# Optimization experiments

Measured on AMD Instinct MI355X. Metric: run time of the kernel, lower is better.

## Reference

```python
import jax, jax.numpy as jnp
import numpy as np

NUM_EXPERTS = 8
TOP_K = 2
INIT_STD = 0.02


def setup_inputs() -> dict:
    key = jax.random.key(0)
    ks = jax.random.split(key, 10)
    B, S, H, I, SI, E = 2, 512, 2048, 1408, 5632, NUM_EXPERTS
    return {
        "hidden_states": jax.random.normal(ks[0], (B, S, H), jnp.float32),
        "gate_w": jax.random.normal(ks[1], (H, E), jnp.float32) * INIT_STD,
        "w_gate": jax.random.normal(ks[2], (E, H, I), jnp.float32) * INIT_STD,
        "w_up": jax.random.normal(ks[3], (E, H, I), jnp.float32) * INIT_STD,
        "w_down": jax.random.normal(ks[4], (E, I, H), jnp.float32) * INIT_STD,
        "sw_gate": jax.random.normal(ks[5], (H, SI), jnp.float32) * INIT_STD,
        "sw_up": jax.random.normal(ks[6], (H, SI), jnp.float32) * INIT_STD,
        "sw_down": jax.random.normal(ks[7], (SI, H), jnp.float32) * INIT_STD,
        "shared_gate_w": jax.random.normal(ks[8], (H, 1), jnp.float32) * INIT_STD,
    }


def reference(hidden_states, gate_w, w_gate, w_up, w_down, sw_gate, sw_up, sw_down, shared_gate_w):
    # Router: logits [B,S,E] in float32, softmax, top-k (norm_topk_prob=False)
    router_logits = (hidden_states @ gate_w).astype(jnp.float32)
    routing_weights = jax.nn.softmax(router_logits, axis=-1)
    top_w, sel = jax.lax.top_k(routing_weights, TOP_K)  # [B,S,K]
    # Scatter top-k weights back to dense per-expert weights [B,S,E]
    # (equals sum_k (sel==e) * top_w, as in the original masked accumulation)
    w = (jax.nn.one_hot(sel, NUM_EXPERTS, dtype=top_w.dtype) * top_w[..., None]).sum(axis=-2)
    # Dense loop over all experts, vectorized as batched einsum (same math)
    g = jnp.einsum('bsh,ehi->bsei', hidden_states, w_gate)
    u = jnp.einsum('bsh,ehi->bsei', hidden_states, w_up)
    expert_out = jnp.einsum('bsei,eih->bseh', jax.nn.silu(g) * u, w_down)  # [B,S,E,H]
    moe_out = jnp.einsum('bse,bseh->bsh', w.astype(hidden_states.dtype), expert_out)
    # Shared expert with sigmoid gate
    shared = (jax.nn.silu(hidden_states @ sw_gate) * (hidden_states @ sw_up)) @ sw_down
    shared = jax.nn.sigmoid(hidden_states @ shared_gate_w) * shared
    return moe_out + shared, router_logits
```

## Files before the change

kernel.cpp:

```cpp
#include <hip/hip_runtime.h>
#include <hip/hip_bf16.h>

#define T_TOK 1024
#define HDIM  2048
#define NEXP  8
#define IDIM  1408
#define SIDIM 5632
#define MAXSLOTS 24

typedef __attribute__((ext_vector_type(8))) short bf16x8;
typedef __attribute__((ext_vector_type(4))) float f32x4;
typedef unsigned short ushort_t;

__device__ __forceinline__ unsigned f2bf(float x) {
    unsigned u = __float_as_uint(x);
    return (u + 0x7fffu + ((u >> 16) & 1u)) >> 16;
}
__device__ __forceinline__ unsigned pack2(float a, float b) {
    return f2bf(a) | (f2bf(b) << 16);
}
__device__ __forceinline__ void async16(const void* g, void* l) {
    __builtin_amdgcn_global_load_lds(
        (const __attribute__((address_space(1))) void*)g,
        (__attribute__((address_space(3))) void*)l, 16, 0, 0);
}

__global__ __launch_bounds__(256) void conv_x(
    const float* __restrict__ src, ushort_t* __restrict__ dst)
{
    const int i = blockIdx.x * 256 + threadIdx.x;
    const float4* s = (const float4*)src + (size_t)i * 2;
    float4 a = s[0], b = s[1];
    union { ushort_t us[8]; uint4 v; } o;
    o.us[0] = (ushort_t)f2bf(a.x); o.us[1] = (ushort_t)f2bf(a.y);
    o.us[2] = (ushort_t)f2bf(a.z); o.us[3] = (ushort_t)f2bf(a.w);
    o.us[4] = (ushort_t)f2bf(b.x); o.us[5] = (ushort_t)f2bf(b.y);
    o.us[6] = (ushort_t)f2bf(b.z); o.us[7] = (ushort_t)f2bf(b.w);
    ((uint4*)dst)[i] = o.v;
}

__global__ __launch_bounds__(256) void conv_all(
    const float* __restrict__ wg, const float* __restrict__ wu,
    const float* __restrict__ wd, const float* __restrict__ swg,
    const float* __restrict__ swu, const float* __restrict__ swd,
    ushort_t* __restrict__ wtg, ushort_t* __restrict__ wtu,
    ushort_t* __restrict__ wtd, ushort_t* __restrict__ swtg,
    ushort_t* __restrict__ swtu, ushort_t* __restrict__ swtd)
{
    int id = blockIdx.x;
    const float* src; ushort_t* dst; int K, N, ktile, ntile;
    if (id < 11264) {
        const float* s0; ushort_t* d0;
        if (id < 5632) { s0 = wg; d0 = wtg; } else { s0 = wu; d0 = wtu; id -= 5632; }
        const int e = id / 704, t = id % 704;
        K = 2048; N = 1408;
        src = s0 + (size_t)e * K * N; dst = d0 + (size_t)e * K * N;
        ntile = t % 22; ktile = t / 22;
    } else if (id < 16896) {
        const int t2 = id - 11264;
        const int e = t2 / 704, t = t2 % 704;
        K = 1408; N = 2048;
        src = wd + (size_t)e * K * N; dst = wtd + (size_t)e * K * N;
        ntile = t % 32; ktile = t / 32;
    } else if (id < 22528) {
        int t2 = id - 16896; const float* s0; ushort_t* d0;
        if (t2 < 2816) { s0 = swg; d0 = swtg; } else { s0 = swu; d0 = swtu; t2 -= 2816; }
        K = 2048; N = 5632;
        src = s0; dst = d0;
        ntile = t2 % 88; ktile = t2 / 88;
    } else {
        const int t2 = id - 22528;
        K = 5632; N = 2048; src = swd; dst = swtd;
        ntile = t2 % 32; ktile = t2 / 32;
    }
    const int tid = threadIdx.x;
    __shared__ __align__(16) unsigned ldsw[32 * 68];
    const float* sp = src + (size_t)(ktile * 64) * N + ntile * 64;
    const int m = tid & 15;
    const int ph = tid >> 4;
#pragma unroll
    for (int h = 0; h < 2; ++h) {
        const int P = ph + h * 16;
        const float* r0 = sp + (size_t)(2 * P) * N + m * 4;
        f32x4 a = __builtin_nontemporal_load((const f32x4*)r0);
        f32x4 b = __builtin_nontemporal_load((const f32x4*)(r0 + N));
        uint4 u;
        u.x = pack2(a[0], b[0]); u.y = pack2(a[1], b[1]);
        u.z = pack2(a[2], b[2]); u.w = pack2(a[3], b[3]);
        *(uint4*)&ldsw[P * 68 + 4 * (m ^ (P >> 2))] = u;
    }
    __syncthreads();
    ushort_t* dp = dst + (size_t)(ntile * 64) * K + ktile * 64;
#pragma unroll
    for (int j = 0; j < 2; ++j) {
        const int c = tid + j * 256;
        const int row = c >> 3, kc = c & 7;
        const int base = 4 * ((row >> 2) ^ kc) + (row & 3);
        uint4 v;
        v.x = ldsw[(4 * kc + 0) * 68 + base];
        v.y = ldsw[(4 * kc + 1) * 68 + base];
        v.z = ldsw[(4 * kc + 2) * 68 + base];
        v.w = ldsw[(4 * kc + 3) * 68 + base];
        *(uint4*)(dp + (size_t)row * K + kc * 8) = v;
    }
}

__global__ __launch_bounds__(256) void router_kernel(
    const float* __restrict__ hs, const float* __restrict__ gw,
    const float* __restrict__ sgw, float* __restrict__ out_logits,
    float* __restrict__ w_dense, float* __restrict__ sgate,
    int* __restrict__ counts, int* __restrict__ tok_list)
{
    const int t = blockIdx.x;
    const int tid = threadIdx.x;
    const float* h = hs + (size_t)t * HDIM;
    float acc[9];
#pragma unroll
    for (int e = 0; e < 9; ++e) acc[e] = 0.f;
    for (int i = tid; i < HDIM; i += 256) {
        float hv = h[i];
        const float4* g4 = (const float4*)(gw + (size_t)i * NEXP);
        float4 g0 = g4[0], g1 = g4[1];
        acc[0] += hv * g0.x; acc[1] += hv * g0.y;
        acc[2] += hv * g0.z; acc[3] += hv * g0.w;
        acc[4] += hv * g1.x; acc[5] += hv * g1.y;
        acc[6] += hv * g1.z; acc[7] += hv * g1.w;
        acc[8] += hv * sgw[i];
    }
#pragma unroll
    for (int e = 0; e < 9; ++e)
        for (int off = 32; off > 0; off >>= 1)
            acc[e] += __shfl_down(acc[e], off, 64);
    __shared__ float lds[4][9];
    const int wid = tid >> 6, lane = tid & 63;
    if (lane == 0)
        for (int e = 0; e < 9; ++e) lds[wid][e] = acc[e];
    __syncthreads();
    if (tid == 0) {
        float l[9];
        for (int e = 0; e < 9; ++e)
            l[e] = lds[0][e] + lds[1][e] + lds[2][e] + lds[3][e];
        for (int e = 0; e < NEXP; ++e) out_logits[(size_t)t * NEXP + e] = l[e];
        float m = l[0];
        for (int e = 1; e < NEXP; ++e) m = fmaxf(m, l[e]);
        float p[NEXP], s = 0.f;
        for (int e = 0; e < NEXP; ++e) { p[e] = expf(l[e] - m); s += p[e]; }
        float inv = 1.f / s;
        for (int e = 0; e < NEXP; ++e) p[e] *= inv;
        int e0 = 0;
        for (int e = 1; e < NEXP; ++e) if (p[e] > p[e0]) e0 = e;
        int e1 = (e0 == 0) ? 1 : 0;
        for (int e = 0; e < NEXP; ++e) if (e != e0 && p[e] > p[e1]) e1 = e;
        for (int e = 0; e < NEXP; ++e)
            w_dense[(size_t)t * NEXP + e] = (e == e0) ? p[e0] : ((e == e1) ? p[e1] : 0.f);
        sgate[t] = 1.f / (1.f + expf(-l[8]));
        int p0 = atomicAdd(&counts[e0], 1); tok_list[e0 * T_TOK + p0] = t;
        int p1 = atomicAdd(&counts[e1], 1); tok_list[e1 * T_TOK + p1] = t;
    }
}

__global__ __launch_bounds__(64) void slot_kernel(
    const int* __restrict__ counts, int* __restrict__ slot_e,
    int* __restrict__ slot_rb, int* __restrict__ nslots)
{
    if (threadIdx.x == 0 && blockIdx.x == 0) {
        int ns = 0;
        for (int e = 0; e < NEXP; ++e)
            for (int b = 0; b < counts[e]; b += 128) {
                slot_e[ns] = e; slot_rb[ns] = b; ++ns;
            }
        nslots[0] = ns;
    }
}

__global__ __launch_bounds__(256) void gateup_all(
    const ushort_t* __restrict__ Xb,
    const ushort_t* __restrict__ swtg, const ushort_t* __restrict__ swtu,
    const ushort_t* __restrict__ wtg, const ushort_t* __restrict__ wtu,
    ushort_t* __restrict__ Ysh, ushort_t* __restrict__ Yr,
    const int* __restrict__ slot_e, const int* __restrict__ slot_rb,
    const int* __restrict__ counts, const int* __restrict__ nslots,
    const int* __restrict__ tok_list, const ushort_t* __restrict__ zerobuf)
{
    const int id = blockIdx.x;
    int n0, slot, e, rowbase, N, mode;
    if (id < 704) {
        mode = 1; n0 = (id % 88) * 64; slot = id / 88; e = 0; rowbase = 0; N = SIDIM;
    } else {
        mode = 0;
        const int id2 = id - 704;
        n0 = (id2 % 22) * 64; slot = id2 / 22;
        if (slot >= nslots[0]) return;
        e = slot_e[slot]; rowbase = slot_rb[slot]; N = IDIM;
    }
    const ushort_t* __restrict__ Wg = mode ? swtg : wtg + (size_t)e * HDIM * IDIM;
    const ushort_t* __restrict__ Wu = mode ? swtu : wtu + (size_t)e * HDIM * IDIM;
    ushort_t* __restrict__ Y = mode ? Ysh : Yr;
    const int K = HDIM;

    const int tid = threadIdx.x, lane = tid & 63, wid = tid >> 6;
    const int wr = (wid >> 1) * 64;
    const int wc = (wid & 1) * 32;
    const int fm = lane & 15, kg = lane >> 4;

    __shared__ int ltok[128];
    __shared__ __align__(16) ushort_t Xa[128 * 64];
    __shared__ __align__(16) ushort_t Bgs[64 * 64];
    __shared__ __align__(16) ushort_t Bus[64 * 64];

    if (tid < 128) {
        int tg;
        if (mode == 0) {
            int cnt = counts[e];
            tg = (rowbase + tid < cnt) ? tok_list[e * T_TOK + rowbase + tid] : -1;
        } else {
            tg = slot * 128 + tid;
        }
        ltok[tid] = tg;
    }
    __syncthreads();

    f32x4 ag[4][2], au[4][2];
#pragma unroll
    for (int a = 0; a < 4; ++a)
#pragma unroll
        for (int b = 0; b < 2; ++b) {
            ag[a][b] = f32x4{0.f, 0.f, 0.f, 0.f};
            au[a][b] = f32x4{0.f, 0.f, 0.f, 0.f};
        }

    const int koff = (((tid & 7) ^ ((tid >> 3) & 7))) * 8;
    const ushort_t* pA[4];
#pragma unroll
    for (int j = 0; j < 4; ++j) {
        const int r = (tid >> 3) + j * 32;
        const int tk = ltok[r];
        pA[j] = (tk >= 0) ? Xb + (size_t)tk * K + koff : zerobuf;
    }
    const ushort_t* pG[2];
    const ushort_t* pU[2];
#pragma unroll
    for (int j = 0; j < 2; ++j) {
        const int r = (tid >> 3) + j * 32;
        pG[j] = Wg + (size_t)(n0 + r) * K + koff;
        pU[j] = Wu + (size_t)(n0 + r) * K + koff;
    }

    for (int k0 = 0; k0 < K; k0 += 64) {
#pragma unroll
        for (int j = 0; j < 4; ++j)
            async16(pA[j] + k0, &Xa[(j * 256 + wid * 64) * 8]);
#pragma unroll
        for (int j = 0; j < 2; ++j) {
            async16(pG[j] + k0, &Bgs[(j * 256 + wid * 64) * 8]);
            async16(pU[j] + k0, &Bus[(j * 256 + wid * 64) * 8]);
        }
        __syncthreads();

#pragma unroll
        for (int ks = 0; ks < 2; ++ks) {
            const int kx = ((ks * 4 + kg) ^ (fm & 7)) * 8;
            bf16x8 af[4];
#pragma unroll
            for (int mt = 0; mt < 4; ++mt)
                af[mt] = *(const bf16x8*)&Xa[(wr + mt * 16 + fm) * 64 + kx];
#pragma unroll
            for (int nt = 0; nt < 2; ++nt) {
                const int rb = (wc + nt * 16 + fm) * 64 + kx;
                bf16x8 bg = *(const bf16x8*)&Bgs[rb];
                bf16x8 bu = *(const bf16x8*)&Bus[rb];
#pragma unroll
                for (int mt = 0; mt < 4; ++mt) {
                    ag[mt][nt] = __builtin_amdgcn_mfma_f32_16x16x32_bf16(af[mt], bg, ag[mt][nt], 0, 0, 0);
                    au[mt][nt] = __builtin_amdgcn_mfma_f32_16x16x32_bf16(af[mt], bu, au[mt][nt], 0, 0, 0);
                }
            }
        }
        __syncthreads();
    }

#pragma unroll
    for (int mt = 0; mt < 4; ++mt)
#pragma unroll
        for (int nt = 0; nt < 2; ++nt) {
            const int col = n0 + wc + nt * 16 + fm;
#pragma unroll
            for (int i = 0; i < 4; ++i) {
                const int row = wr + mt * 16 + kg * 4 + i;
                float g = ag[mt][nt][i], u = au[mt][nt][i];
                float yv = g / (1.f + expf(-g)) * u;
                Y[(size_t)(slot * 128 + row) * N + col] = (ushort_t)f2bf(yv);
            }
        }
}

__global__ __launch_bounds__(256) void down_all(
    const ushort_t* __restrict__ Ysh, const ushort_t* __restrict__ Yr,
    const ushort_t* __restrict__ swtd, const ushort_t* __restrict__ wtd,
    float* __restrict__ out,
    const int* __restrict__ slot_e, const int* __restrict__ slot_rb,
    const int* __restrict__ counts, const int* __restrict__ nslots,
    const int* __restrict__ tok_list, const float* __restrict__ w_dense,
    const float* __restrict__ sgate)
{
    const int id = blockIdx.x;
    int n0, slot, e, rowbase, K, kbase, ksteps, mode;
    const ushort_t* Yb;
    const ushort_t* Wd;
    if (id < 512) {
        mode = 1;
        n0 = (id & 15) * 128; slot = (id >> 4) & 7;
        const int z = id >> 7;
        K = SIDIM; kbase = z * 1408; ksteps = 22;
        e = 0; rowbase = 0;
        Yb = Ysh + (size_t)slot * 128 * K;
        Wd = swtd;
    } else {
        mode = 0;
        const int id2 = id - 512;
        n0 = (id2 & 15) * 128;
        const int rest = id2 >> 4;
        slot = rest >> 1;
        if (slot >= nslots[0]) return;
        const int z = rest & 1;
        K = IDIM; kbase = z * 704; ksteps = 11;
        e = slot_e[slot]; rowbase = slot_rb[slot];
        Yb = Yr + (size_t)slot * 128 * K;
        Wd = wtd + (size_t)e * IDIM * HDIM;
    }
    const int tid = threadIdx.x, lane = tid & 63, wid = tid >> 6;
    const int wr = (wid >> 1) * 64;
    const int wc = (wid & 1) * 64;
    const int fm = lane & 15, kg = lane >> 4;

    __shared__ int ltok[128];
    __shared__ float lw[128];
    __shared__ __align__(16) ushort_t Ya[128 * 64];
    __shared__ __align__(16) ushort_t Bd[128 * 64];

    if (tid < 128) {
        int tg; float wv;
        if (mode == 0) {
            int cnt = counts[e];
            if (rowbase + tid < cnt) {
                tg = tok_list[e * T_TOK + rowbase + tid];
                wv = w_dense[(size_t)tg * NEXP + e];
            } else { tg = -1; wv = 0.f; }
        } else {
            tg = slot * 128 + tid; wv = sgate[tg];
        }
        ltok[tid] = tg; lw[tid] = wv;
    }
    __syncthreads();

    f32x4 acc[4][4];
#pragma unroll
    for (int a = 0; a < 4; ++a)
#pragma unroll
        for (int b = 0; b < 4; ++b) acc[a][b] = f32x4{0.f, 0.f, 0.f, 0.f};

    const int koff = (((tid & 7) ^ ((tid >> 3) & 7))) * 8;
    const ushort_t* pY[4];
    const ushort_t* pW[4];
#pragma unroll
    for (int j = 0; j < 4; ++j) {
        const int r = (tid >> 3) + j * 32;
        pY[j] = Yb + (size_t)r * K + kbase + koff;
        pW[j] = Wd + (size_t)(n0 + r) * K + kbase + koff;
    }

    for (int s = 0; s < ksteps; ++s) {
        const int k0 = s * 64;
#pragma unroll
        for (int j = 0; j < 4; ++j) {
            async16(pY[j] + k0, &Ya[(j * 256 + wid * 64) * 8]);
            async16(pW[j] + k0, &Bd[(j * 256 + wid * 64) * 8]);
        }
        __syncthreads();

#pragma unroll
        for (int ks = 0; ks < 2; ++ks) {
            const int kx = ((ks * 4 + kg) ^ (fm & 7)) * 8;
            bf16x8 af[4];
#pragma unroll
            for (int mt = 0; mt < 4; ++mt)
                af[mt] = *(const bf16x8*)&Ya[(wr + mt * 16 + fm) * 64 + kx];
#pragma unroll
            for (int nt = 0; nt < 4; ++nt) {
                bf16x8 bf = *(const bf16x8*)&Bd[(wc + nt * 16 + fm) * 64 + kx];
#pragma unroll
                for (int mt = 0; mt < 4; ++mt)
                    acc[mt][nt] = __builtin_amdgcn_mfma_f32_16x16x32_bf16(af[mt], bf, acc[mt][nt], 0, 0, 0);
            }
        }
        __syncthreads();
    }

#pragma unroll
    for (int mt = 0; mt < 4; ++mt)
#pragma unroll
        for (int nt = 0; nt < 4; ++nt) {
            const int col = n0 + wc + nt * 16 + fm;
#pragma unroll
            for (int i = 0; i < 4; ++i) {
                const int row = wr + mt * 16 + kg * 4 + i;
                const int tg = ltok[row];
                if (tg >= 0)
                    atomicAdd(out + (size_t)tg * HDIM + col, lw[row] * acc[mt][nt][i]);
            }
        }
}

extern "C" void kernel_launch(void* const* d_in, const int* in_sizes, int n_in,
                              void* d_out, int out_size, void* d_ws, size_t ws_size,
                              hipStream_t stream)
{
    const float* hs  = (const float*)d_in[0];
    const float* gw  = (const float*)d_in[1];
    const float* wg  = (const float*)d_in[2];
    const float* wu  = (const float*)d_in[3];
    const float* wd  = (const float*)d_in[4];
    const float* swg = (const float*)d_in[5];
    const float* swu = (const float*)d_in[6];
    const float* swd = (const float*)d_in[7];
    const float* sgw = (const float*)d_in[8];
    float* out = (float*)d_out;
    char* ws = (char*)d_ws;

    float* w_dense      = (float*)(ws + 0x00000);
    float* sgate        = (float*)(ws + 0x08000);
    int* counts         = (int*)(ws + 0x09000);
    int* nslots         = (int*)(ws + 0x09100);
    int* slot_e         = (int*)(ws + 0x09200);
    int* slot_rb        = (int*)(ws + 0x09300);
    int* tok_list       = (int*)(ws + 0x09400);
    ushort_t* zerobuf   = (ushort_t*)(ws + 0x11400);
    ushort_t* Xb        = (ushort_t*)(ws + 0x20000);
    ushort_t* Yr        = (ushort_t*)(ws + 0x420000);
    ushort_t* Ysh       = (ushort_t*)(ws + 0xC60000);
    ushort_t* wtg       = (ushort_t*)(ws + 0x1760000);
    ushort_t* wtu       = (ushort_t*)(ws + 0x4360000);
    ushort_t* wtd       = (ushort_t*)(ws + 0x6F60000);
    ushort_t* swtg      = (ushort_t*)(ws + 0x9B60000);
    ushort_t* swtu      = (ushort_t*)(ws + 0xB160000);
    ushort_t* swtd      = (ushort_t*)(ws + 0xC760000);
    float* out_logits = out + (size_t)T_TOK * HDIM;

    hipMemsetAsync(counts, 0, 256, stream);
    hipMemsetAsync(zerobuf, 0, 16384, stream);
    hipMemsetAsync(out, 0, (size_t)T_TOK * HDIM * sizeof(float), stream);

    conv_x<<<dim3(1024), dim3(256), 0, stream>>>(hs, Xb);
    conv_all<<<dim3(25344), dim3(256), 0, stream>>>(
        wg, wu, wd, swg, swu, swd, wtg, wtu, wtd, swtg, swtu, swtd);

    router_kernel<<<dim3(T_TOK), dim3(256), 0, stream>>>(
        hs, gw, sgw, out_logits, w_dense, sgate, counts, tok_list);
    slot_kernel<<<dim3(1), dim3(64), 0, stream>>>(counts, slot_e, slot_rb, nslots);

    gateup_all<<<dim3(704 + 22 * MAXSLOTS), dim3(256), 0, stream>>>(
        Xb, swtg, swtu, wtg, wtu, Ysh, Yr,
        slot_e, slot_rb, counts, nslots, tok_list, zerobuf);

    down_all<<<dim3(512 + 16 * MAXSLOTS * 2), dim3(256), 0, stream>>>(
        Ysh, Yr, swtd, wtd, out,
        slot_e, slot_rb, counts, nslots, tok_list, w_dense, sgate);
}
```

Measured before the change: 585.6 us.

## Double-buffer LDS tiles in gate-up and down MoE GEMM kernels

Both GEMM kernels now keep two LDS buffers for the activation and weight tiles. The async global-to-LDS copy for the next K-step is issued before the MFMA work on the current step, so load latency can overlap compute instead of being serialized behind a barrier. This doubles per-block shared memory to about 64 KB in each kernel, which can reduce how many blocks fit on a CU at once.

```diff
diff --git a/kernel.cpp b/kernel.cpp
--- a/kernel.cpp
+++ b/kernel.cpp
@@ -204,9 +204,9 @@
     const int fm = lane & 15, kg = lane >> 4;
 
     __shared__ int ltok[128];
-    __shared__ __align__(16) ushort_t Xa[128 * 64];
-    __shared__ __align__(16) ushort_t Bgs[64 * 64];
-    __shared__ __align__(16) ushort_t Bus[64 * 64];
+    __shared__ __align__(16) ushort_t Xa[2][128 * 64];
+    __shared__ __align__(16) ushort_t Bgs[2][64 * 64];
+    __shared__ __align__(16) ushort_t Bus[2][64 * 64];
 
     if (tid < 128) {
         int tg;
@@ -246,16 +246,25 @@
         pU[j] = Wu + (size_t)(n0 + r) * K + koff;
     }
 
-    for (int k0 = 0; k0 < K; k0 += 64) {
-#pragma unroll
-        for (int j = 0; j < 4; ++j)
-            async16(pA[j] + k0, &Xa[(j * 256 + wid * 64) * 8]);
-#pragma unroll
-        for (int j = 0; j < 2; ++j) {
-            async16(pG[j] + k0, &Bgs[(j * 256 + wid * 64) * 8]);
-            async16(pU[j] + k0, &Bus[(j * 256 + wid * 64) * 8]);
-        }
-        __syncthreads();
+#define STAGE_GU(buf, k0)                                                   \
+    {                                                                       \
+        _Pragma("unroll")                                                   \
+        for (int j = 0; j < 4; ++j)                                         \
+            async16(pA[j] + (k0), &Xa[buf][(j * 256 + wid * 64) * 8]);      \
+        _Pragma("unroll")                                                   \
+        for (int j = 0; j < 2; ++j) {                                       \
+            async16(pG[j] + (k0), &Bgs[buf][(j * 256 + wid * 64) * 8]);     \
+            async16(pU[j] + (k0), &Bus[buf][(j * 256 + wid * 64) * 8]);     \
+        }                                                                   \
+    }
+
+    const int NT = K / 64;
+    STAGE_GU(0, 0);
+    __syncthreads();
+
+    for (int t = 0; t < NT; ++t) {
+        const int cur = t & 1;
+        if (t + 1 < NT) STAGE_GU(cur ^ 1, (t + 1) * 64);
 
 #pragma unroll
         for (int ks = 0; ks < 2; ++ks) {
@@ -263,12 +272,12 @@
             bf16x8 af[4];
 #pragma unroll
             for (int mt = 0; mt < 4; ++mt)
-                af[mt] = *(const bf16x8*)&Xa[(wr + mt * 16 + fm) * 64 + kx];
+                af[mt] = *(const bf16x8*)&Xa[cur][(wr + mt * 16 + fm) * 64 + kx];
 #pragma unroll
             for (int nt = 0; nt < 2; ++nt) {
                 const int rb = (wc + nt * 16 + fm) * 64 + kx;
-                bf16x8 bg = *(const bf16x8*)&Bgs[rb];
-                bf16x8 bu = *(const bf16x8*)&Bus[rb];
+                bf16x8 bg = *(const bf16x8*)&Bgs[cur][rb];
+                bf16x8 bu = *(const bf16x8*)&Bus[cur][rb];
 #pragma unroll
                 for (int mt = 0; mt < 4; ++mt) {
                     ag[mt][nt] = __builtin_amdgcn_mfma_f32_16x16x32_bf16(af[mt], bg, ag[mt][nt], 0, 0, 0);
@@ -278,6 +287,7 @@
         }
         __syncthreads();
     }
+#undef STAGE_GU
 
 #pragma unroll
     for (int mt = 0; mt < 4; ++mt)
@@ -335,8 +345,8 @@
 
     __shared__ int ltok[128];
     __shared__ float lw[128];
-    __shared__ __align__(16) ushort_t Ya[128 * 64];
-    __shared__ __align__(16) ushort_t Bd[128 * 64];
+    __shared__ __align__(16) ushort_t Ya[2][128 * 64];
+    __shared__ __align__(16) ushort_t Bd[2][128 * 64];
 
     if (tid < 128) {
         int tg; float wv;
@@ -369,14 +379,21 @@
         pW[j] = Wd + (size_t)(n0 + r) * K + kbase + koff;
     }
 
+#define STAGE_D(buf, k0)                                                    \
+    {                                                                       \
+        _Pragma("unroll")                                                   \
+        for (int j = 0; j < 4; ++j) {                                       \
+            async16(pY[j] + (k0), &Ya[buf][(j * 256 + wid * 64) * 8]);      \
+            async16(pW[j] + (k0), &Bd[buf][(j * 256 + wid * 64) * 8]);      \
+        }                                                                   \
+    }
+
+    STAGE_D(0, 0);
+    __syncthreads();
+
     for (int s = 0; s < ksteps; ++s) {
-        const int k0 = s * 64;
-#pragma unroll
-        for (int j = 0; j < 4; ++j) {
-            async16(pY[j] + k0, &Ya[(j * 256 + wid * 64) * 8]);
-            async16(pW[j] + k0, &Bd[(j * 256 + wid * 64) * 8]);
-        }
-        __syncthreads();
+        const int cur = s & 1;
+        if (s + 1 < ksteps) STAGE_D(cur ^ 1, (s + 1) * 64);
 
 #pragma unroll
         for (int ks = 0; ks < 2; ++ks) {
@@ -384,10 +401,10 @@
             bf16x8 af[4];
 #pragma unroll
             for (int mt = 0; mt < 4; ++mt)
-                af[mt] = *(const bf16x8*)&Ya[(wr + mt * 16 + fm) * 64 + kx];
+                af[mt] = *(const bf16x8*)&Ya[cur][(wr + mt * 16 + fm) * 64 + kx];
 #pragma unroll
             for (int nt = 0; nt < 4; ++nt) {
-                bf16x8 bf = *(const bf16x8*)&Bd[(wc + nt * 16 + fm) * 64 + kx];
+                bf16x8 bf = *(const bf16x8*)&Bd[cur][(wc + nt * 16 + fm) * 64 + kx];
 #pragma unroll
                 for (int mt = 0; mt < 4; ++mt)
                     acc[mt][nt] = __builtin_amdgcn_mfma_f32_16x16x32_bf16(af[mt], bf, acc[mt][nt], 0, 0, 0);
@@ -395,6 +412,7 @@
         }
         __syncthreads();
     }
+#undef STAGE_D
 
 #pragma unroll
     for (int mt = 0; mt < 4; ++mt)
```

New measurement: 639.0 us. 1.09x slower.
